# Optimization experiments

Hardware: AMD Instinct MI355X
Metric: run time of the kernel (lower is better)

The kernel has to match this reference:

```python
import jax, jax.numpy as jnp
import numpy as np

EPS = 0.001          # sinkhorn_args['eps']
MAX_ITERS = 100      # sinkhorn_args['max_iters'] (torch early-stops at a fixed point;
                     # running all iters yields the same converged values within tol)


def setup_inputs() -> dict:
    key = jax.random.key(0)
    B, N, d_in, n_ref = 64, 2048, 128, 256
    X = jax.random.normal(key, (B, N, d_in), dtype=jnp.float32)
    # uniform_ref = linspace(-1,1,n_ref) repeated across d_in (the learned parameter's init)
    reference = jnp.tile(jnp.linspace(-1.0, 1.0, n_ref, dtype=jnp.float32)[:, None], (1, d_in))
    return {"X": X, "reference": reference}


def _cdist(a, b):
    # Euclidean pairwise distance (p=2) via gram trick; avoids B x n x m x d blowup.
    a2 = jnp.sum(a * a, axis=-1)[:, :, None]   # (B, n, 1)
    b2 = jnp.sum(b * b, axis=-1)[:, None, :]   # (B, 1, m)
    sq = a2 + b2 - 2.0 * jnp.einsum("bnd,bmd->bnm", a, b)
    return jnp.sqrt(jnp.maximum(sq, 0.0))


def reference(X, reference):
    B, N, d = X.shape
    n_ref = reference.shape[0]
    ref_b = jnp.broadcast_to(reference[None], (B, n_ref, d))
    C = _cdist(ref_b, X)                       # (B, n_ref, N)
    # uniform weights -> scalar log-weights
    log_wx = jnp.log(1.0 / n_ref + 1e-8)
    log_wy = jnp.log(1.0 / N + 1e-8)

    def step(carry, _):
        u, v = carry
        u = EPS * (log_wx - jax.nn.logsumexp((-C + v[:, None, :]) / EPS, axis=2))
        v = EPS * (log_wy - jax.nn.logsumexp((-C + u[:, :, None]) / EPS, axis=1))
        return (u, v), None

    u0 = jnp.zeros((B, n_ref), dtype=C.dtype)
    v0 = jnp.zeros((B, N), dtype=C.dtype)
    (u, v), _ = jax.lax.scan(step, (u0, v0), None, length=MAX_ITERS)

    P = jnp.exp((-C + u[:, :, None] + v[:, None, :]) / EPS)   # transport plan (B, n_ref, N)
    denom = jnp.sum(P, axis=2, keepdims=True) + 1e-8
    barycenters = jnp.einsum("bnm,bmd->bnd", P, X) / denom
    return barycenters - reference[None]       # (B, n_ref, d_in)
```

## Files before the change

kernel.cpp:

```cpp
#include <hip/hip_runtime.h>
#include <math.h>

#define BATCH 64
#define NREF  256
#define NPTS  2048
#define DIM   128
#define ITERS 100
#define INV_EPS 1000.0f
#define RCHUNK 8
#define NCHUNK (NREF / RCHUNK)


__global__ __launch_bounds__(256) void cgemm_kernel(const float* __restrict__ X,
                                                    const float* __restrict__ ref,
                                                    float* __restrict__ C) {
    __shared__ float rs[8 * 128];
    __shared__ float xs[8 * 128];
    __shared__ float r2s[128];
    __shared__ float x2s[128];
    int b  = blockIdx.x >> 5;
    int it = (blockIdx.x >> 4) & 1;
    int jt = blockIdx.x & 15;
    int i0 = it * 128, j0 = jt * 128;
    int t  = threadIdx.x;
    int ti = t >> 4, tj = t & 15;

    int sr = t >> 1;
    int sh = (t & 1) * 4;
    const float* refp = ref + (size_t)(i0 + sr) * DIM + sh;
    const float* xp   = X + ((size_t)b * NPTS + j0 + sr) * DIM + sh;

    float4 acc[2][2][4];
#pragma unroll
    for (int p = 0; p < 2; ++p)
#pragma unroll
        for (int q = 0; q < 2; ++q)
#pragma unroll
            for (int ii = 0; ii < 4; ++ii)
                acc[p][q][ii] = make_float4(0.f, 0.f, 0.f, 0.f);
    float rsq = 0.f, xsq = 0.f;

    for (int k0 = 0; k0 < DIM; k0 += 8) {
        float4 rv = *(const float4*)(refp + k0);
        float4 xv = *(const float4*)(xp + k0);
        rsq += rv.x * rv.x + rv.y * rv.y + rv.z * rv.z + rv.w * rv.w;
        xsq += xv.x * xv.x + xv.y * xv.y + xv.z * xv.z + xv.w * xv.w;
        __syncthreads();
        rs[(sh + 0) * 128 + sr] = rv.x; rs[(sh + 1) * 128 + sr] = rv.y;
        rs[(sh + 2) * 128 + sr] = rv.z; rs[(sh + 3) * 128 + sr] = rv.w;
        xs[(sh + 0) * 128 + sr] = xv.x; xs[(sh + 1) * 128 + sr] = xv.y;
        xs[(sh + 2) * 128 + sr] = xv.z; xs[(sh + 3) * 128 + sr] = xv.w;
        __syncthreads();

        const float4* rs4 = (const float4*)rs;
        const float4* xs4 = (const float4*)xs;
#pragma unroll
        for (int k = 0; k < 8; ++k) {
            float4 a0 = rs4[k * 32 + ti];
            float4 a1 = rs4[k * 32 + 16 + ti];
            float4 b0 = xs4[k * 32 + tj];
            float4 b1 = xs4[k * 32 + 16 + tj];
#define FMA4(ACC, S, BV)                                                     \
            ACC.x = fmaf(S, BV.x, ACC.x); ACC.y = fmaf(S, BV.y, ACC.y);      \
            ACC.z = fmaf(S, BV.z, ACC.z); ACC.w = fmaf(S, BV.w, ACC.w);
#define ROW(P, S, II)                                                        \
            FMA4(acc[P][0][II], S, b0) FMA4(acc[P][1][II], S, b1)
            ROW(0, a0.x, 0) ROW(0, a0.y, 1) ROW(0, a0.z, 2) ROW(0, a0.w, 3)
            ROW(1, a1.x, 0) ROW(1, a1.y, 1) ROW(1, a1.z, 2) ROW(1, a1.w, 3)
#undef ROW
#undef FMA4
        }
    }

    rsq += __shfl_xor(rsq, 1);
    xsq += __shfl_xor(xsq, 1);
    if ((t & 1) == 0) { r2s[sr] = rsq; x2s[sr] = xsq; }
    __syncthreads();

    float x2v[2][4];
#pragma unroll
    for (int q = 0; q < 2; ++q)
#pragma unroll
        for (int e = 0; e < 4; ++e)
            x2v[q][e] = x2s[q * 64 + tj * 4 + e];

#pragma unroll
    for (int p = 0; p < 2; ++p)
#pragma unroll
        for (int ii = 0; ii < 4; ++ii) {
            int il = p * 64 + ti * 4 + ii;
            float rr = r2s[il];
            float* crow = C + ((size_t)b * NREF + i0 + il) * NPTS + j0;
#pragma unroll
            for (int q = 0; q < 2; ++q) {
                float4 av = acc[p][q][ii];
                float4 o;
                o.x = sqrtf(fmaxf(rr + x2v[q][0] - 2.f * av.x, 0.f)) * INV_EPS;
                o.y = sqrtf(fmaxf(rr + x2v[q][1] - 2.f * av.y, 0.f)) * INV_EPS;
                o.z = sqrtf(fmaxf(rr + x2v[q][2] - 2.f * av.z, 0.f)) * INV_EPS;
                o.w = sqrtf(fmaxf(rr + x2v[q][3] - 2.f * av.w, 0.f)) * INV_EPS;
                *(float4*)(crow + q * 64 + tj * 4) = o;
            }
        }
}

__global__ __launch_bounds__(512, 3) void uv_kernel(const float* __restrict__ C,
                                                    const float* __restrict__ v,
                                                    float* __restrict__ u,
                                                    float* __restrict__ Pl,
                                                    float log_wx) {
    __shared__ float smx[RCHUNK][8];
    __shared__ float sms[RCHUNK][8];
    int b     = blockIdx.x >> 5;
    int chunk = blockIdx.x & 31;
    int t     = threadIdx.x;
    int lane  = t & 63;
    int w     = t >> 6;

    const float* Cb = C + (size_t)(b * NREF + chunk * RCHUNK) * NPTS;
    float4 vj = *(const float4*)(v + (size_t)b * NPTS + 4 * t);

    float4 a[RCHUNK];
#pragma unroll
    for (int i = 0; i < RCHUNK; ++i)
        a[i] = *(const float4*)(Cb + (size_t)i * NPTS + 4 * t);

    float m[RCHUNK], su[RCHUNK];
#pragma unroll
    for (int i = 0; i < RCHUNK; ++i) {
        a[i].x = vj.x - a[i].x; a[i].y = vj.y - a[i].y;
        a[i].z = vj.z - a[i].z; a[i].w = vj.w - a[i].w;
        m[i] = fmaxf(fmaxf(a[i].x, a[i].y), fmaxf(a[i].z, a[i].w));
    }
#pragma unroll
    for (int i = 0; i < RCHUNK; ++i)
#pragma unroll
        for (int off = 1; off < 64; off <<= 1)
            m[i] = fmaxf(m[i], __shfl_xor(m[i], off));
    if (lane == 0) {
#pragma unroll
        for (int i = 0; i < RCHUNK; ++i) smx[i][w] = m[i];
    }
    __syncthreads();
#pragma unroll
    for (int i = 0; i < RCHUNK; ++i) {
        float mm = smx[i][0];
#pragma unroll
        for (int q = 1; q < 8; ++q) mm = fmaxf(mm, smx[i][q]);
        m[i] = mm;
    }
#pragma unroll
    for (int i = 0; i < RCHUNK; ++i)
        su[i] = __expf(a[i].x - m[i]) + __expf(a[i].y - m[i])
              + __expf(a[i].z - m[i]) + __expf(a[i].w - m[i]);
#pragma unroll
    for (int i = 0; i < RCHUNK; ++i)
#pragma unroll
        for (int off = 1; off < 64; off <<= 1)
            su[i] += __shfl_xor(su[i], off);
    if (lane == 0) {
#pragma unroll
        for (int i = 0; i < RCHUNK; ++i) sms[i][w] = su[i];
    }
    __syncthreads();
#pragma unroll
    for (int i = 0; i < RCHUNK; ++i) {
        float s = ((sms[i][0] + sms[i][1]) + (sms[i][2] + sms[i][3]))
                + ((sms[i][4] + sms[i][5]) + (sms[i][6] + sms[i][7]));
        su[i] = log_wx - (m[i] + __logf(s));
    }
    int ub = b * NREF + chunk * RCHUNK;
#pragma unroll
    for (int i = 0; i < RCHUNK; ++i)
        if (t == i) u[ub + i] = su[i];

    float4 pl;
#define COLL(Q)                                                              \
    {                                                                        \
        float mq = a[0].Q + su[0];                                           \
        _Pragma("unroll")                                                    \
        for (int i_ = 1; i_ < RCHUNK; ++i_)                                  \
            mq = fmaxf(mq, a[i_].Q + su[i_]);                                \
        float sq_ = 0.f;                                                     \
        _Pragma("unroll")                                                    \
        for (int i_ = 0; i_ < RCHUNK; ++i_)                                  \
            sq_ += __expf(a[i_].Q + su[i_] - mq);                            \
        pl.Q = (mq - vj.Q) + __logf(sq_);                                    \
    }
    COLL(x) COLL(y) COLL(z) COLL(w)
#undef COLL
    *(float4*)(Pl + (size_t)(b * NCHUNK + chunk) * NPTS + 4 * t) = pl;
}

__global__ __launch_bounds__(256) void vmerge_kernel(const float* __restrict__ Pl,
                                                     float* __restrict__ v,
                                                     float log_wy) {
    int b = blockIdx.x >> 3;
    int j = ((blockIdx.x & 7) << 8) + threadIdx.x;
    const float* p = Pl + (size_t)b * NCHUNK * NPTS + j;
    float l[NCHUNK];
#pragma unroll
    for (int c = 0; c < NCHUNK; ++c) l[c] = p[(size_t)c * NPTS];
    float m = l[0];
#pragma unroll
    for (int c = 1; c < NCHUNK; ++c) m = fmaxf(m, l[c]);
    float s = 0.f;
#pragma unroll
    for (int c = 0; c < NCHUNK; ++c) s += __expf(l[c] - m);
    v[(size_t)b * NPTS + j] = log_wy - (m + __logf(s));
}

__global__ __launch_bounds__(512, 2) void out_partialA(const float* __restrict__ C,
                                                       const float* __restrict__ X,
                                                       const float* __restrict__ u,
                                                       const float* __restrict__ v,
                                                       float* __restrict__ Np,
                                                       float* __restrict__ denp) {
    __shared__ float wts[NREF * 16];
    __shared__ float xt[16 * DIM];
    int b  = blockIdx.x >> 3;
    int jc = blockIdx.x & 7;
    int j0 = jc * 256;
    int t  = threadIdx.x;
    int s  = t & 15;
    int g  = t >> 4;

    const float* Cb = C + (size_t)b * NREF * NPTS + j0;
    const float* ub = u + b * NREF;
    const float* vb = v + (size_t)b * NPTS + j0;

    float4 a0[8], a1[8];
    float ws[8];
#pragma unroll
    for (int r = 0; r < 8; ++r) {
        a0[r] = make_float4(0.f, 0.f, 0.f, 0.f);
        a1[r] = make_float4(0.f, 0.f, 0.f, 0.f);
        ws[r] = 0.f;
    }

    for (int jt = 0; jt < 256; jt += 16) {
#pragma unroll
        for (int k = 0; k < 2; ++k) {
            int fidx = t + 512 * k;
            int r = fidx >> 2, q = fidx & 3;
            float4 cv = *(const float4*)(Cb + (size_t)r * NPTS + jt + 4 * q);
            float4 vv = *(const float4*)(vb + jt + 4 * q);
            float uu = ub[r];
            float4 wv;
            wv.x = __expf(uu + vv.x - cv.x);
            wv.y = __expf(uu + vv.y - cv.y);
            wv.z = __expf(uu + vv.z - cv.z);
            wv.w = __expf(uu + vv.w - cv.w);
            int sw = q ^ ((r >> 3) & 3);
            *(float4*)&wts[r * 16 + sw * 4] = wv;
        }
        const float4* Xb4 = (const float4*)(X + ((size_t)b * NPTS + j0 + jt) * DIM);
        ((float4*)xt)[t] = Xb4[t];
        __syncthreads();

        const float4* xt4 = (const float4*)xt;
#pragma unroll 2
        for (int jp = 0; jp < 8; ++jp) {
            int j1 = 2 * jp;
            float4 xa0 = xt4[j1 * 32 + s];
            float4 xa1 = xt4[j1 * 32 + 16 + s];
            float4 xb0 = xt4[(j1 + 1) * 32 + s];
            float4 xb1 = xt4[(j1 + 1) * 32 + 16 + s];
            int q   = jp >> 1;
            int h   = jp & 1;
            int swb = (q ^ (g & 3)) * 4 + 2 * h;
#pragma unroll
            for (int rr = 0; rr < 8; ++rr) {
                int r = g * 8 + rr;
                float2 w2 = *(const float2*)&wts[r * 16 + swb];
                a0[rr].x = fmaf(w2.x, xa0.x, a0[rr].x);
                a0[rr].y = fmaf(w2.x, xa0.y, a0[rr].y);
                a0[rr].z = fmaf(w2.x, xa0.z, a0[rr].z);
                a0[rr].w = fmaf(w2.x, xa0.w, a0[rr].w);
                a1[rr].x = fmaf(w2.x, xa1.x, a1[rr].x);
                a1[rr].y = fmaf(w2.x, xa1.y, a1[rr].y);
                a1[rr].z = fmaf(w2.x, xa1.z, a1[rr].z);
                a1[rr].w = fmaf(w2.x, xa1.w, a1[rr].w);
                a0[rr].x = fmaf(w2.y, xb0.x, a0[rr].x);
                a0[rr].y = fmaf(w2.y, xb0.y, a0[rr].y);
                a0[rr].z = fmaf(w2.y, xb0.z, a0[rr].z);
                a0[rr].w = fmaf(w2.y, xb0.w, a0[rr].w);
                a1[rr].x = fmaf(w2.y, xb1.x, a1[rr].x);
                a1[rr].y = fmaf(w2.y, xb1.y, a1[rr].y);
                a1[rr].z = fmaf(w2.y, xb1.z, a1[rr].z);
                a1[rr].w = fmaf(w2.y, xb1.w, a1[rr].w);
                ws[rr] += w2.x + w2.y;
            }
        }
        __syncthreads();
    }

    float* npb = Np + ((size_t)jc * BATCH * NREF + (size_t)b * NREF) * DIM;
#pragma unroll
    for (int rr = 0; rr < 8; ++rr) {
        int r = g * 8 + rr;
        float4* nrow = (float4*)(npb + (size_t)r * DIM);
        nrow[s]      = a0[rr];
        nrow[16 + s] = a1[rr];
        if (s == 0) denp[(size_t)jc * BATCH * NREF + b * NREF + r] = ws[rr];
    }
}

__global__ __launch_bounds__(256) void out_finishA(const float* __restrict__ Np,
                                                   const float* __restrict__ denp,
                                                   const float* __restrict__ ref,
                                                   float* __restrict__ out) {
    const int NPL  = BATCH * NREF * DIM / 4;
    const int DENP = BATCH * NREF;
    int fidx = blockIdx.x * 256 + threadIdx.x;
    int bi   = fidx >> 5;
    float4 n4 = make_float4(0.f, 0.f, 0.f, 0.f);
    float dn = 0.f;
    const float4* np4 = (const float4*)Np;
#pragma unroll
    for (int jc = 0; jc < 8; ++jc) {
        float4 p = np4[(size_t)jc * NPL + fidx];
        n4.x += p.x; n4.y += p.y; n4.z += p.z; n4.w += p.w;
        dn += denp[(size_t)jc * DENP + bi];
    }
    float inv = 1.0f / (dn + 1e-8f);
    int i = bi & 255;
    int q = fidx & 31;
    float4 rf = ((const float4*)ref)[i * 32 + q];
    float4 o;
    o.x = n4.x * inv - rf.x;
    o.y = n4.y * inv - rf.y;
    o.z = n4.z * inv - rf.z;
    o.w = n4.w * inv - rf.w;
    ((float4*)out)[fidx] = o;
}

__global__ __launch_bounds__(256) void out_kernelB(const float* __restrict__ C,
                                                   const float* __restrict__ X,
                                                   const float* __restrict__ ref,
                                                   const float* __restrict__ u,
                                                   const float* __restrict__ v,
                                                   float* __restrict__ out) {
    __shared__ float wt[32 * 32];
    __shared__ float xt[32 * DIM];
    int b  = blockIdx.x >> 3;
    int it = blockIdx.x & 7;
    int i0 = it * 32;
    int t  = threadIdx.x;
    int s  = t & 31;
    int g  = t >> 5;

    const float* Cb = C + ((size_t)b * NREF + i0) * NPTS;
    const float* vb = v + (size_t)b * NPTS;
    const float* ub = u + (size_t)b * NREF + i0;

    float4 acc[4];
    float wsum[4];
#pragma unroll
    for (int r = 0; r < 4; ++r) { acc[r] = make_float4(0.f, 0.f, 0.f, 0.f); wsum[r] = 0.f; }

    for (int j0 = 0; j0 < NPTS; j0 += 32) {
#pragma unroll
        for (int k = 0; k < 4; ++k) {
            int widx = t + 256 * k;
            int r    = widx >> 5;
            int jj   = widx & 31;
            wt[widx] = __expf(ub[r] + vb[j0 + jj] - Cb[(size_t)r * NPTS + j0 + jj]);
        }
        const float4* Xb4 = (const float4*)(X + ((size_t)b * NPTS + j0) * DIM);
#pragma unroll
        for (int k = 0; k < 4; ++k) {
            int idx = t + 256 * k;
            ((float4*)xt)[idx] = Xb4[idx];
        }
        __syncthreads();

        const float4* xt4 = (const float4*)xt;
#pragma unroll 2
        for (int jj = 0; jj < 32; jj += 4) {
            float4 xv0 = xt4[(jj + 0) * 32 + s];
            float4 xv1 = xt4[(jj + 1) * 32 + s];
            float4 xv2 = xt4[(jj + 2) * 32 + s];
            float4 xv3 = xt4[(jj + 3) * 32 + s];
#pragma unroll
            for (int r = 0; r < 4; ++r) {
                float4 w4 = *(const float4*)&wt[(g * 4 + r) * 32 + jj];
                acc[r].x = fmaf(w4.x, xv0.x, acc[r].x); acc[r].y = fmaf(w4.x, xv0.y, acc[r].y);
                acc[r].z = fmaf(w4.x, xv0.z, acc[r].z); acc[r].w = fmaf(w4.x, xv0.w, acc[r].w);
                acc[r].x = fmaf(w4.y, xv1.x, acc[r].x); acc[r].y = fmaf(w4.y, xv1.y, acc[r].y);
                acc[r].z = fmaf(w4.y, xv1.z, acc[r].z); acc[r].w = fmaf(w4.y, xv1.w, acc[r].w);
                acc[r].x = fmaf(w4.z, xv2.x, acc[r].x); acc[r].y = fmaf(w4.z, xv2.y, acc[r].y);
                acc[r].z = fmaf(w4.z, xv2.z, acc[r].z); acc[r].w = fmaf(w4.z, xv2.w, acc[r].w);
                acc[r].x = fmaf(w4.w, xv3.x, acc[r].x); acc[r].y = fmaf(w4.w, xv3.y, acc[r].y);
                acc[r].z = fmaf(w4.w, xv3.z, acc[r].z); acc[r].w = fmaf(w4.w, xv3.w, acc[r].w);
                wsum[r] += (w4.x + w4.y) + (w4.z + w4.w);
            }
        }
        __syncthreads();
    }

#pragma unroll
    for (int r = 0; r < 4; ++r) {
        int i = i0 + g * 4 + r;
        float dn = wsum[r] + 1e-8f;
        float inv = 1.0f / dn;
        float4 rf = ((const float4*)(ref + (size_t)i * DIM))[s];
        float4 o;
        o.x = acc[r].x * inv - rf.x;
        o.y = acc[r].y * inv - rf.y;
        o.z = acc[r].z * inv - rf.z;
        o.w = acc[r].w * inv - rf.w;
        ((float4*)(out + ((size_t)b * NREF + i) * DIM))[s] = o;
    }
}

extern "C" void kernel_launch(void* const* d_in, const int* in_sizes, int n_in,
                              void* d_out, int out_size, void* d_ws, size_t ws_size,
                              hipStream_t stream) {
    const float* X   = (const float*)d_in[0];
    const float* ref = (const float*)d_in[1];
    float* out = (float*)d_out;

    char* ws = (char*)d_ws;
    size_t o = 0;
    float* C = (float*)(ws + o); o += (size_t)BATCH * NREF * NPTS * sizeof(float);
    float* u = (float*)(ws + o); o += (size_t)BATCH * NREF * sizeof(float);
    float* v = (float*)(ws + o); o += (size_t)BATCH * NPTS * sizeof(float);
    float* Pl = (float*)(ws + o);
    float* Np = (float*)(ws + o);
    size_t oA = o + (size_t)8 * BATCH * NREF * DIM * sizeof(float);
    float* denp = (float*)(ws + oA);
    oA += (size_t)8 * BATCH * NREF * sizeof(float);
    bool bigws = (ws_size >= oA);

    const float log_wx = (float)log(1.0 / (double)NREF + 1e-8);
    const float log_wy = (float)log(1.0 / (double)NPTS + 1e-8);

    hipMemsetAsync(v, 0, (size_t)BATCH * NPTS * sizeof(float), stream);

    cgemm_kernel<<<BATCH * 32, 256, 0, stream>>>(X, ref, C);

    for (int t = 0; t < ITERS; ++t) {
        uv_kernel<<<BATCH * NCHUNK, 512, 0, stream>>>(C, v, u, Pl, log_wx);
        vmerge_kernel<<<BATCH * NPTS / 256, 256, 0, stream>>>(Pl, v, log_wy);
    }

    if (bigws) {
        out_partialA<<<BATCH * 8, 512, 0, stream>>>(C, X, u, v, Np, denp);
        out_finishA<<<BATCH * NREF * DIM / 1024, 256, 0, stream>>>(Np, denp, ref, out);
    } else {
        out_kernelB<<<BATCH * 8, 256, 0, stream>>>(C, X, ref, u, v, out);
    }
}
```

Baseline: 3.957 ms.

## Merge more reference rows per uv block with online logsumexp to shrink partials

Each uv_kernel block now covers 16 reference rows, processed as four sub-chunks of 4. The column-wise log-sum-exp is carried across sub-chunks as an online running max and sum. This halves the number of per-column partials written to Pl and later read by vmerge_kernel, which cuts memory traffic on every Sinkhorn iteration. Register pressure per sub-chunk drops, so the occupancy hint goes from 3 to 4. The cost is half as many blocks in the grid, extra synchronisation inside the sub-chunk loop, and extra exp calls for the rescaling.

```diff
diff --git a/kernel.cpp b/kernel.cpp
--- a/kernel.cpp
+++ b/kernel.cpp
@@ -7,8 +7,9 @@
 #define DIM   128
 #define ITERS 100
 #define INV_EPS 1000.0f
-#define RCHUNK 8
-#define NCHUNK (NREF / RCHUNK)
+#define RCH    4
+#define NSUB   4
+#define NCHUNK 16
 
 
 __global__ __launch_bounds__(256) void cgemm_kernel(const float* __restrict__ X,
@@ -104,92 +105,103 @@
         }
 }
 
-__global__ __launch_bounds__(512, 3) void uv_kernel(const float* __restrict__ C,
+__global__ __launch_bounds__(512, 4) void uv_kernel(const float* __restrict__ C,
                                                     const float* __restrict__ v,
                                                     float* __restrict__ u,
                                                     float* __restrict__ Pl,
                                                     float log_wx) {
-    __shared__ float smx[RCHUNK][8];
-    __shared__ float sms[RCHUNK][8];
-    int b     = blockIdx.x >> 5;
-    int chunk = blockIdx.x & 31;
-    int t     = threadIdx.x;
-    int lane  = t & 63;
-    int w     = t >> 6;
-
-    const float* Cb = C + (size_t)(b * NREF + chunk * RCHUNK) * NPTS;
+    __shared__ float smx[RCH][8];
+    __shared__ float sms[RCH][8];
+    int b    = blockIdx.x >> 4;
+    int co   = blockIdx.x & 15;
+    int t    = threadIdx.x;
+    int lane = t & 63;
+    int w    = t >> 6;
+
     float4 vj = *(const float4*)(v + (size_t)b * NPTS + 4 * t);
-
-    float4 a[RCHUNK];
-#pragma unroll
-    for (int i = 0; i < RCHUNK; ++i)
-        a[i] = *(const float4*)(Cb + (size_t)i * NPTS + 4 * t);
-
-    float m[RCHUNK], su[RCHUNK];
-#pragma unroll
-    for (int i = 0; i < RCHUNK; ++i) {
-        a[i].x = vj.x - a[i].x; a[i].y = vj.y - a[i].y;
-        a[i].z = vj.z - a[i].z; a[i].w = vj.w - a[i].w;
-        m[i] = fmaxf(fmaxf(a[i].x, a[i].y), fmaxf(a[i].z, a[i].w));
-    }
-#pragma unroll
-    for (int i = 0; i < RCHUNK; ++i)
-#pragma unroll
-        for (int off = 1; off < 64; off <<= 1)
-            m[i] = fmaxf(m[i], __shfl_xor(m[i], off));
-    if (lane == 0) {
-#pragma unroll
-        for (int i = 0; i < RCHUNK; ++i) smx[i][w] = m[i];
-    }
-    __syncthreads();
-#pragma unroll
-    for (int i = 0; i < RCHUNK; ++i) {
-        float mm = smx[i][0];
-#pragma unroll
-        for (int q = 1; q < 8; ++q) mm = fmaxf(mm, smx[i][q]);
-        m[i] = mm;
-    }
-#pragma unroll
-    for (int i = 0; i < RCHUNK; ++i)
-        su[i] = __expf(a[i].x - m[i]) + __expf(a[i].y - m[i])
-              + __expf(a[i].z - m[i]) + __expf(a[i].w - m[i]);
-#pragma unroll
-    for (int i = 0; i < RCHUNK; ++i)
-#pragma unroll
-        for (int off = 1; off < 64; off <<= 1)
-            su[i] += __shfl_xor(su[i], off);
-    if (lane == 0) {
-#pragma unroll
-        for (int i = 0; i < RCHUNK; ++i) sms[i][w] = su[i];
-    }
-    __syncthreads();
-#pragma unroll
-    for (int i = 0; i < RCHUNK; ++i) {
-        float s = ((sms[i][0] + sms[i][1]) + (sms[i][2] + sms[i][3]))
-                + ((sms[i][4] + sms[i][5]) + (sms[i][6] + sms[i][7]));
-        su[i] = log_wx - (m[i] + __logf(s));
-    }
-    int ub = b * NREF + chunk * RCHUNK;
-#pragma unroll
-    for (int i = 0; i < RCHUNK; ++i)
-        if (t == i) u[ub + i] = su[i];
+    float4 pm = make_float4(-INFINITY, -INFINITY, -INFINITY, -INFINITY);
+    float4 ps = make_float4(0.f, 0.f, 0.f, 0.f);
+
+    for (int cc = 0; cc < NSUB; ++cc) {
+        int r0 = co * (RCH * NSUB) + cc * RCH;
+        const float* Cb = C + (size_t)(b * NREF + r0) * NPTS;
+
+        float4 a[RCH];
+#pragma unroll
+        for (int i = 0; i < RCH; ++i)
+            a[i] = *(const float4*)(Cb + (size_t)i * NPTS + 4 * t);
+
+        float m[RCH], su[RCH];
+#pragma unroll
+        for (int i = 0; i < RCH; ++i) {
+            a[i].x = vj.x - a[i].x; a[i].y = vj.y - a[i].y;
+            a[i].z = vj.z - a[i].z; a[i].w = vj.w - a[i].w;
+            m[i] = fmaxf(fmaxf(a[i].x, a[i].y), fmaxf(a[i].z, a[i].w));
+        }
+#pragma unroll
+        for (int i = 0; i < RCH; ++i)
+#pragma unroll
+            for (int off = 1; off < 64; off <<= 1)
+                m[i] = fmaxf(m[i], __shfl_xor(m[i], off));
+        if (lane == 0) {
+#pragma unroll
+            for (int i = 0; i < RCH; ++i) smx[i][w] = m[i];
+        }
+        __syncthreads();
+#pragma unroll
+        for (int i = 0; i < RCH; ++i) {
+            float mm = smx[i][0];
+#pragma unroll
+            for (int q = 1; q < 8; ++q) mm = fmaxf(mm, smx[i][q]);
+            m[i] = mm;
+        }
+#pragma unroll
+        for (int i = 0; i < RCH; ++i)
+            su[i] = __expf(a[i].x - m[i]) + __expf(a[i].y - m[i])
+                  + __expf(a[i].z - m[i]) + __expf(a[i].w - m[i]);
+#pragma unroll
+        for (int i = 0; i < RCH; ++i)
+#pragma unroll
+            for (int off = 1; off < 64; off <<= 1)
+                su[i] += __shfl_xor(su[i], off);
+        if (lane == 0) {
+#pragma unroll
+            for (int i = 0; i < RCH; ++i) sms[i][w] = su[i];
+        }
+        __syncthreads();
+#pragma unroll
+        for (int i = 0; i < RCH; ++i) {
+            float s = ((sms[i][0] + sms[i][1]) + (sms[i][2] + sms[i][3]))
+                    + ((sms[i][4] + sms[i][5]) + (sms[i][6] + sms[i][7]));
+            su[i] = log_wx - (m[i] + __logf(s));
+        }
+#pragma unroll
+        for (int i = 0; i < RCH; ++i)
+            if (t == i) u[b * NREF + r0 + i] = su[i];
+
+#define CMERGE(Q)                                                            \
+        {                                                                    \
+            float mq = a[0].Q + su[0];                                       \
+            _Pragma("unroll")                                                \
+            for (int i_ = 1; i_ < RCH; ++i_)                                 \
+                mq = fmaxf(mq, a[i_].Q + su[i_]);                            \
+            float nm = fmaxf(pm.Q, mq);                                      \
+            float sq_ = ps.Q * __expf(pm.Q - nm);                            \
+            _Pragma("unroll")                                                \
+            for (int i_ = 0; i_ < RCH; ++i_)                                 \
+                sq_ += __expf(a[i_].Q + su[i_] - nm);                        \
+            pm.Q = nm; ps.Q = sq_;                                           \
+        }
+        CMERGE(x) CMERGE(y) CMERGE(z) CMERGE(w)
+#undef CMERGE
+    }
 
     float4 pl;
-#define COLL(Q)                                                              \
-    {                                                                        \
-        float mq = a[0].Q + su[0];                                           \
-        _Pragma("unroll")                                                    \
-        for (int i_ = 1; i_ < RCHUNK; ++i_)                                  \
-            mq = fmaxf(mq, a[i_].Q + su[i_]);                                \
-        float sq_ = 0.f;                                                     \
-        _Pragma("unroll")                                                    \
-        for (int i_ = 0; i_ < RCHUNK; ++i_)                                  \
-            sq_ += __expf(a[i_].Q + su[i_] - mq);                            \
-        pl.Q = (mq - vj.Q) + __logf(sq_);                                    \
-    }
-    COLL(x) COLL(y) COLL(z) COLL(w)
-#undef COLL
-    *(float4*)(Pl + (size_t)(b * NCHUNK + chunk) * NPTS + 4 * t) = pl;
+    pl.x = (pm.x - vj.x) + __logf(ps.x);
+    pl.y = (pm.y - vj.y) + __logf(ps.y);
+    pl.z = (pm.z - vj.z) + __logf(ps.z);
+    pl.w = (pm.w - vj.w) + __logf(ps.w);
+    *(float4*)(Pl + (size_t)(b * NCHUNK + co) * NPTS + 4 * t) = pl;
 }
 
 __global__ __launch_bounds__(256) void vmerge_kernel(const float* __restrict__ Pl,
```

Result: no change. 3.945 ms (-0.3%).
